# Performance work log

Measured on AMD Instinct MI355X. Metric: run time of the kernel, lower is better.

Reference implementation:

```python
import jax, jax.numpy as jnp
import numpy as np
from math import pi

N_, C_, H_, W_, S_ = 32, 3, 224, 224, 16  # batch, channels, height, width, n_samples
INIT_VALUE = pi * 30 / 180.0  # dataset 'imagenet_r30' -> rotations in +-30 degrees


def setup_inputs() -> dict:
    key = jax.random.key(0)
    k1, k2 = jax.random.split(key)
    x = jax.random.normal(k1, (N_, C_, H_, W_), jnp.float32)
    # torch: cat((zeros(N), rand(N*S)*2-1)) * init_value, reshaped per-image: col 0 is identity
    u = jax.random.uniform(k2, (N_, S_), jnp.float32) * 2.0 - 1.0
    thetas = jnp.concatenate([jnp.zeros((N_, 1), jnp.float32), u * INIT_VALUE], axis=1)
    return {"x": x, "thetas": thetas}


def _rotation_grid(thetas, H, W, dtype):
    # F.affine_grid(align_corners=False): pixel-center normalized coords
    xs = ((jnp.arange(W, dtype=dtype) + 0.5) * 2.0 / W - 1.0)  # [W]
    ys = ((jnp.arange(H, dtype=dtype) + 0.5) * 2.0 / H - 1.0)  # [H]
    c = jnp.cos(thetas)[..., None, None]  # [N,S1,1,1]
    s = jnp.sin(thetas)[..., None, None]
    # theta matrix [[c,-s,0],[s,c,0]] applied to (x, y, 1)
    gx = c * xs[None, :] - s * ys[:, None]  # [N,S1,H,W]
    gy = s * xs[None, :] + c * ys[:, None]
    return gx, gy


def _grid_sample_bilinear_zeros(img, gx, gy):
    # img: [C,H,W]; gx,gy: [S1,H,W] normalized coords; align_corners=False, zero padding
    C, H, W = img.shape
    ix = ((gx + 1.0) * W - 1.0) * 0.5
    iy = ((gy + 1.0) * H - 1.0) * 0.5
    ix0f = jnp.floor(ix)
    iy0f = jnp.floor(iy)
    wx1 = ix - ix0f
    wy1 = iy - iy0f
    wx0 = 1.0 - wx1
    wy0 = 1.0 - wy1
    ix0 = ix0f.astype(jnp.int32)
    iy0 = iy0f.astype(jnp.int32)
    ix1 = ix0 + 1
    iy1 = iy0 + 1

    def gather(iy_, ix_, w):
        valid = (ix_ >= 0) & (ix_ < W) & (iy_ >= 0) & (iy_ < H)
        v = img[:, jnp.clip(iy_, 0, H - 1), jnp.clip(ix_, 0, W - 1)]  # [C,S1,H,W]
        return v * (w * valid.astype(img.dtype))[None]

    out = (gather(iy0, ix0, wy0 * wx0) + gather(iy0, ix1, wy0 * wx1)
           + gather(iy1, ix0, wy1 * wx0) + gather(iy1, ix1, wy1 * wx1))
    return jnp.transpose(out, (1, 0, 2, 3))  # [S1,C,H,W]


def reference(x, thetas):
    N, C, H, W = x.shape
    gx, gy = _rotation_grid(thetas, H, W, x.dtype)  # [N,S1,H,W] each
    out = jax.vmap(_grid_sample_bilinear_zeros)(x, gx, gy)  # [N,S1,C,H,W]
    return out
```

## Files before the change

kernel.cpp:

```cpp
#include <hip/hip_runtime.h>
#include <math.h>

namespace {
constexpr int N_  = 32;
constexpr int S1_ = 17;
constexpr int C_  = 3;
constexpr int H_  = 224;
constexpr int W_  = 224;
constexpr int HW_ = H_ * W_;
constexpr int TILE = 32;
constexpr int TPL  = W_ / TILE;
constexpr int LH   = 46;
constexpr int LWX  = 48;
constexpr int LSTR = 49;
constexpr int THREADS = 256;
}

__global__ __launch_bounds__(THREADS) void rot_bilinear_lds_kernel(
    const float* __restrict__ x,
    const float* __restrict__ thetas,
    float* __restrict__ out) {
  __shared__ float lds[C_][LH * LSTR];

  const int ns = blockIdx.y;
  const int n  = ns / S1_;
  const int bx = blockIdx.x;
  const int h0 = (bx / TPL) * TILE;
  const int w0 = (bx % TPL) * TILE;

  const float theta = thetas[ns];
  float st, ct;
  sincosf(theta, &st, &ct);

  float fxmin = 1e30f, fymin = 1e30f;
#pragma unroll
  for (int cw = 0; cw < 2; ++cw) {
#pragma unroll
    for (int chh = 0; chh < 2; ++chh) {
      const float xs = ((w0 + cw * (TILE - 1)) + 0.5f) * (2.0f / W_) - 1.0f;
      const float ys = ((h0 + chh * (TILE - 1)) + 0.5f) * (2.0f / H_) - 1.0f;
      const float gx = ct * xs - st * ys;
      const float gy = st * xs + ct * ys;
      const float fx = ((gx + 1.0f) * W_ - 1.0f) * 0.5f;
      const float fy = ((gy + 1.0f) * H_ - 1.0f) * 0.5f;
      fxmin = fminf(fxmin, fx);
      fymin = fminf(fymin, fy);
    }
  }
  int rx0 = (int)floorf(fxmin - 0.1f);
  const int ry0 = (int)floorf(fymin - 0.1f);
  rx0 &= ~1;

  const float* __restrict__ img = x + (size_t)n * (C_ * HW_);
  const int tid = threadIdx.x;
  const bool interior =
      (rx0 >= 0) & (ry0 >= 0) & (rx0 + LWX <= W_) & (ry0 + LH <= H_);
  if (interior) {
    const float* __restrict__ p0 = img + ry0 * W_ + rx0;
    constexpr int NPAIR = LH * (LWX / 2);
    for (int i = tid; i < NPAIR; i += THREADS) {
      const int r  = i / (LWX / 2);
      const int c2 = i - r * (LWX / 2);
      const int go = r * W_ + 2 * c2;
      const int lo = r * LSTR + 2 * c2;
      const float2 v0 = *reinterpret_cast<const float2*>(p0 + go);
      const float2 v1 = *reinterpret_cast<const float2*>(p0 + HW_ + go);
      const float2 v2 = *reinterpret_cast<const float2*>(p0 + 2 * HW_ + go);
      lds[0][lo] = v0.x; lds[0][lo + 1] = v0.y;
      lds[1][lo] = v1.x; lds[1][lo + 1] = v1.y;
      lds[2][lo] = v2.x; lds[2][lo + 1] = v2.y;
    }
  } else {
    for (int i = tid; i < LH * LWX; i += THREADS) {
      const int r = i / LWX;
      const int c = i - r * LWX;
      const int gy = ry0 + r;
      const int gx = rx0 + c;
      const bool in = (gx >= 0) & (gx < W_) & (gy >= 0) & (gy < H_);
      const int off = (in ? gy : 0) * W_ + (in ? gx : 0);
      const float m = in ? 1.0f : 0.0f;
      const int lo = r * LSTR + c;
      lds[0][lo] = img[off] * m;
      lds[1][lo] = img[HW_ + off] * m;
      lds[2][lo] = img[2 * HW_ + off] * m;
    }
  }
  __syncthreads();

  const int row = tid >> 3;
  const int col = (tid & 7) * 4;
  const int h = h0 + row;
  const int w_base = w0 + col;
  const float ys = (h + 0.5f) * (2.0f / H_) - 1.0f;
  const float xs0 = (w_base + 0.5f) * (2.0f / W_) - 1.0f;
  const float gx0 = ct * xs0 - st * ys;
  const float gy0 = st * xs0 + ct * ys;
  float fx = ((gx0 + 1.0f) * W_ - 1.0f) * 0.5f;
  float fy = ((gy0 + 1.0f) * H_ - 1.0f) * 0.5f;

  float r0[4], r1[4], r2[4];
#pragma unroll
  for (int k = 0; k < 4; ++k) {
    const float fx0 = floorf(fx);
    const float fy0 = floorf(fy);
    const float wx1 = fx - fx0;
    const float wy1 = fy - fy0;
    const float wx0 = 1.0f - wx1;
    const float wy0 = 1.0f - wy1;
    const int lx = (int)fx0 - rx0;
    const int ly = (int)fy0 - ry0;
    const int base = ly * LSTR + lx;
    const float w00 = wy0 * wx0, w01 = wy0 * wx1;
    const float w10 = wy1 * wx0, w11 = wy1 * wx1;
    r0[k] = w00 * lds[0][base]        + w01 * lds[0][base + 1] +
            w10 * lds[0][base + LSTR] + w11 * lds[0][base + LSTR + 1];
    r1[k] = w00 * lds[1][base]        + w01 * lds[1][base + 1] +
            w10 * lds[1][base + LSTR] + w11 * lds[1][base + LSTR + 1];
    r2[k] = w00 * lds[2][base]        + w01 * lds[2][base + 1] +
            w10 * lds[2][base + LSTR] + w11 * lds[2][base + LSTR + 1];
    fx += ct;
    fy += st;
  }

  float* __restrict__ o = out + (size_t)ns * (C_ * HW_) + (size_t)h * W_ + w_base;
  *reinterpret_cast<float4*>(o)            = make_float4(r0[0], r0[1], r0[2], r0[3]);
  *reinterpret_cast<float4*>(o + HW_)      = make_float4(r1[0], r1[1], r1[2], r1[3]);
  *reinterpret_cast<float4*>(o + 2 * HW_)  = make_float4(r2[0], r2[1], r2[2], r2[3]);
}

extern "C" void kernel_launch(void* const* d_in, const int* in_sizes, int n_in,
                              void* d_out, int out_size, void* d_ws,
                              size_t ws_size, hipStream_t stream) {
  const float* x      = (const float*)d_in[0];
  const float* thetas = (const float*)d_in[1];
  float* out          = (float*)d_out;

  dim3 grid(TPL * TPL, N_ * S1_);
  rot_bilinear_lds_kernel<<<grid, THREADS, 0, stream>>>(x, thetas, out);
}
```

Baseline: 404.3 us.

## Split channels across blocks to shrink LDS and raise occupancy

Each block now handles a single channel instead of all three, so the grid triples and the LDS tile shrinks to one channel. The LDS stride becomes even, which allows float2 stores into shared memory. The aim is more resident blocks per CU and fewer registers per thread. In exchange, the per-block setup (sincos, bounds, sync) runs three times as often and neighbouring blocks may read the same image rows separately.

Measured after the change: 435.7 us. 7.8% more time.

```diff
diff --git a/kernel.cpp b/kernel.cpp
--- a/kernel.cpp
+++ b/kernel.cpp
@@ -12,7 +12,7 @@
 constexpr int TPL  = W_ / TILE;
 constexpr int LH   = 46;
 constexpr int LWX  = 48;
-constexpr int LSTR = 49;
+constexpr int LSTR = 50;
 constexpr int THREADS = 256;
 }
 
@@ -20,13 +20,15 @@
     const float* __restrict__ x,
     const float* __restrict__ thetas,
     float* __restrict__ out) {
-  __shared__ float lds[C_][LH * LSTR];
+  __shared__ float lds[LH * LSTR];
 
   const int ns = blockIdx.y;
   const int n  = ns / S1_;
   const int bx = blockIdx.x;
-  const int h0 = (bx / TPL) * TILE;
-  const int w0 = (bx % TPL) * TILE;
+  const int c  = bx % C_;
+  const int t  = bx / C_;
+  const int h0 = (t / TPL) * TILE;
+  const int w0 = (t % TPL) * TILE;
 
   const float theta = thetas[ns];
   float st, ct;
@@ -51,7 +53,7 @@
   const int ry0 = (int)floorf(fymin - 0.1f);
   rx0 &= ~1;
 
-  const float* __restrict__ img = x + (size_t)n * (C_ * HW_);
+  const float* __restrict__ img = x + (size_t)n * (C_ * HW_) + (size_t)c * HW_;
   const int tid = threadIdx.x;
   const bool interior =
       (rx0 >= 0) & (ry0 >= 0) & (rx0 + LWX <= W_) & (ry0 + LH <= H_);
@@ -61,28 +63,19 @@
     for (int i = tid; i < NPAIR; i += THREADS) {
       const int r  = i / (LWX / 2);
       const int c2 = i - r * (LWX / 2);
-      const int go = r * W_ + 2 * c2;
-      const int lo = r * LSTR + 2 * c2;
-      const float2 v0 = *reinterpret_cast<const float2*>(p0 + go);
-      const float2 v1 = *reinterpret_cast<const float2*>(p0 + HW_ + go);
-      const float2 v2 = *reinterpret_cast<const float2*>(p0 + 2 * HW_ + go);
-      lds[0][lo] = v0.x; lds[0][lo + 1] = v0.y;
-      lds[1][lo] = v1.x; lds[1][lo + 1] = v1.y;
-      lds[2][lo] = v2.x; lds[2][lo + 1] = v2.y;
+      const float2 v = *reinterpret_cast<const float2*>(p0 + r * W_ + 2 * c2);
+      *reinterpret_cast<float2*>(&lds[r * LSTR + 2 * c2]) = v;
     }
   } else {
     for (int i = tid; i < LH * LWX; i += THREADS) {
       const int r = i / LWX;
-      const int c = i - r * LWX;
+      const int cc = i - r * LWX;
       const int gy = ry0 + r;
-      const int gx = rx0 + c;
+      const int gx = rx0 + cc;
       const bool in = (gx >= 0) & (gx < W_) & (gy >= 0) & (gy < H_);
       const int off = (in ? gy : 0) * W_ + (in ? gx : 0);
       const float m = in ? 1.0f : 0.0f;
-      const int lo = r * LSTR + c;
-      lds[0][lo] = img[off] * m;
-      lds[1][lo] = img[HW_ + off] * m;
-      lds[2][lo] = img[2 * HW_ + off] * m;
+      lds[r * LSTR + cc] = img[off] * m;
     }
   }
   __syncthreads();
@@ -98,7 +91,7 @@
   float fx = ((gx0 + 1.0f) * W_ - 1.0f) * 0.5f;
   float fy = ((gy0 + 1.0f) * H_ - 1.0f) * 0.5f;
 
-  float r0[4], r1[4], r2[4];
+  float r0[4];
 #pragma unroll
   for (int k = 0; k < 4; ++k) {
     const float fx0 = floorf(fx);
@@ -112,20 +105,15 @@
     const int base = ly * LSTR + lx;
     const float w00 = wy0 * wx0, w01 = wy0 * wx1;
     const float w10 = wy1 * wx0, w11 = wy1 * wx1;
-    r0[k] = w00 * lds[0][base]        + w01 * lds[0][base + 1] +
-            w10 * lds[0][base + LSTR] + w11 * lds[0][base + LSTR + 1];
-    r1[k] = w00 * lds[1][base]        + w01 * lds[1][base + 1] +
-            w10 * lds[1][base + LSTR] + w11 * lds[1][base + LSTR + 1];
-    r2[k] = w00 * lds[2][base]        + w01 * lds[2][base + 1] +
-            w10 * lds[2][base + LSTR] + w11 * lds[2][base + LSTR + 1];
+    r0[k] = w00 * lds[base]        + w01 * lds[base + 1] +
+            w10 * lds[base + LSTR] + w11 * lds[base + LSTR + 1];
     fx += ct;
     fy += st;
   }
 
-  float* __restrict__ o = out + (size_t)ns * (C_ * HW_) + (size_t)h * W_ + w_base;
-  *reinterpret_cast<float4*>(o)            = make_float4(r0[0], r0[1], r0[2], r0[3]);
-  *reinterpret_cast<float4*>(o + HW_)      = make_float4(r1[0], r1[1], r1[2], r1[3]);
-  *reinterpret_cast<float4*>(o + 2 * HW_)  = make_float4(r2[0], r2[1], r2[2], r2[3]);
+  float* __restrict__ o = out + (size_t)ns * (C_ * HW_) + (size_t)c * HW_ +
+                          (size_t)h * W_ + w_base;
+  *reinterpret_cast<float4*>(o) = make_float4(r0[0], r0[1], r0[2], r0[3]);
 }
 
 extern "C" void kernel_launch(void* const* d_in, const int* in_sizes, int n_in,
@@ -135,6 +123,6 @@
   const float* thetas = (const float*)d_in[1];
   float* out          = (float*)d_out;
 
-  dim3 grid(TPL * TPL, N_ * S1_);
+  dim3 grid(TPL * TPL * C_, N_ * S1_);
   rot_bilinear_lds_kernel<<<grid, THREADS, 0, stream>>>(x, thetas, out);
 }
```
